# Performance work log

Measured on AMD Instinct MI355X. Metric: run time of the kernel, lower is better.

## Reference

```python
import jax, jax.numpy as jnp
import numpy as np

B, S = 32, 4096
QRYDIM, CTXDIM, ENCDIM = 512, 512, 256


def setup_inputs() -> dict:
    key = jax.random.key(0)
    ks = jax.random.split(key, 8)
    qry = jax.random.normal(ks[0], (B, QRYDIM), dtype=jnp.float32)
    ctx = jax.random.normal(ks[1], (B, S, CTXDIM), dtype=jnp.float32)
    ctx_mask = jax.random.randint(ks[2], (B, S), 0, 2, dtype=jnp.int32)
    # first Linear(qrydim+ctxdim, encdim): split into ctx-part and qry-part
    # (equivalent to concat([ctx, qry]) @ W1^T since concat order is [ctx, qry])
    sc1 = 1.0 / np.sqrt(QRYDIM + CTXDIM)
    Wc = jax.random.uniform(ks[3], (CTXDIM, ENCDIM), jnp.float32, -sc1, sc1)
    Wq = jax.random.uniform(ks[4], (QRYDIM, ENCDIM), jnp.float32, -sc1, sc1)
    b1 = jax.random.uniform(ks[5], (ENCDIM,), jnp.float32, -sc1, sc1)
    sc2 = 1.0 / np.sqrt(ENCDIM)
    w2 = jax.random.uniform(ks[6], (ENCDIM,), jnp.float32, -sc2, sc2)
    b2 = jax.random.uniform(ks[7], (), jnp.float32, -sc2, sc2)
    return {"qry": qry, "ctx": ctx, "ctx_mask": ctx_mask,
            "Wc": Wc, "Wq": Wq, "b1": b1, "w2": w2, "b2": b2}


def reference(qry, ctx, ctx_mask, Wc, Wq, b1, w2, b2):
    # hidden = tanh(concat([ctx, qry_broadcast]) @ W1 + b1), computed without
    # materializing the (B, S, CTXDIM+QRYDIM) concat tensor
    h_ctx = jnp.einsum('bsc,ce->bse', ctx, Wc)          # (B, S, E)
    h_qry = jnp.einsum('bq,qe->be', qry, Wq)            # (B, E)
    h = jnp.tanh(h_ctx + h_qry[:, None, :] + b1)        # (B, S, E)
    scores = jnp.einsum('bse,e->bs', h, w2) + b2        # (B, S)
    # additive log-mask, then softmax over seqlen
    scores = scores + jnp.log(ctx_mask.astype(jnp.float32))
    alphas = jax.nn.softmax(scores, axis=-1)            # (B, S)
    # weighted sum over context (values default to ctx)
    summary = jnp.einsum('bs,bsd->bd', alphas, ctx)     # (B, CTXDIM)
    return alphas, summary, scores
```

## Files before the change

kernel.cpp:

```cpp
#include <hip/hip_runtime.h>
#include <math.h>

#define BB 32
#define SS 4096
#define CD 512
#define ED 256

#define ALPHAS_OFF 0
#define SUMMARY_OFF (BB * SS)
#define SCORES_OFF (BB * SS + BB * CD)

#define NEG_BIG (-1.0e30f)

typedef __attribute__((ext_vector_type(8))) short short8;
typedef __attribute__((ext_vector_type(8))) unsigned short us8;
typedef __attribute__((ext_vector_type(4))) float f32x4;

__device__ __forceinline__ unsigned short f2bf(float f) {
    unsigned u = __float_as_uint(f);
    u += 0x7FFFu + ((u >> 16) & 1u);
    return (unsigned short)(u >> 16);
}
__device__ __forceinline__ float bf2f(unsigned short h) {
    return __uint_as_float(((unsigned)h) << 16);
}
__device__ __forceinline__ float fast_tanh(float x) {
    const float ex = __expf(2.0f * x);
    return 1.0f - __fdividef(2.0f, ex + 1.0f);
}

#define WS_BH_OFF 32768
#define BPLANE 131072

__global__ void k_prep(const float* __restrict__ Wc, unsigned short* __restrict__ Bh,
                       unsigned short* __restrict__ Bl) {
    const int bid = blockIdx.x;
    const int l = threadIdx.x;
    const int e = (bid & 15) * 16 + (l & 15);
    const int kbase = (bid >> 4) * 32 + (l >> 4) * 8;
    const size_t off = ((size_t)bid * 64 + l) * 8;
#pragma unroll
    for (int j = 0; j < 8; ++j) {
        const float f = Wc[(size_t)(kbase + j) * ED + e];
        const unsigned short h = f2bf(f);
        Bh[off + j] = h;
        Bl[off + j] = f2bf(f - bf2f(h));
    }
}

__global__ void k_hq(const float* __restrict__ qry, const float* __restrict__ Wq,
                     const float* __restrict__ b1, float* __restrict__ hq) {
    const int b = blockIdx.x;
    const int e = threadIdx.x;
    __shared__ float qs[CD];
    qs[e] = qry[b * CD + e];
    qs[e + 256] = qry[b * CD + e + 256];
    __syncthreads();
    float acc = b1[e];
#pragma unroll 8
    for (int c = 0; c < CD; ++c) {
        acc = fmaf(qs[c], Wq[c * ED + e], acc);
    }
    hq[b * ED + e] = acc;
}

#define ST 64
__global__ __launch_bounds__(256, 3)
void k_scores(const float* __restrict__ ctx,
              const unsigned short* __restrict__ Bh, const unsigned short* __restrict__ Bl,
              const float* __restrict__ hq, const float* __restrict__ w2,
              const float* __restrict__ b2p, const int* __restrict__ mask,
              float* __restrict__ out) {
    const int b = blockIdx.y;
    const int s0 = blockIdx.x * ST;
    const int tid = threadIdx.x;
    const int w = tid >> 6;
    const int l = tid & 63;
    const int ehalf = w & 1;
    const int mhalf = w >> 1;

    __shared__ unsigned short AsH[4 * 64 * 8];
    __shared__ unsigned short AsL[4 * 64 * 8];
    __shared__ unsigned short BsH[16 * 64 * 8];
    __shared__ unsigned short BsL[16 * 64 * 8];
    __shared__ float red[2][ST];

    f32x4 acc[2][8];
#pragma unroll
    for (int mi = 0; mi < 2; ++mi)
#pragma unroll
        for (int t = 0; t < 8; ++t) acc[mi][t] = (f32x4)(0.0f);

    const float* ctx_b = ctx + (size_t)(b * SS + s0) * CD;

    for (int c = 0; c < 16; ++c) {
        __syncthreads();
#pragma unroll
        for (int i = 0; i < 2; ++i) {
            const int f = tid + i * 256;
            const int r = f >> 3;
            const int kk = (f & 7) * 4;
            const float4 v = *(const float4*)(ctx_b + (size_t)r * CD + c * 32 + kk);
            const unsigned short h0 = f2bf(v.x), h1 = f2bf(v.y), h2 = f2bf(v.z), h3 = f2bf(v.w);
            const ushort4 hv = make_ushort4(h0, h1, h2, h3);
            const ushort4 lv = make_ushort4(f2bf(v.x - bf2f(h0)), f2bf(v.y - bf2f(h1)),
                                            f2bf(v.z - bf2f(h2)), f2bf(v.w - bf2f(h3)));
            const int off = (((r >> 4) * 64) + (r & 15) + 16 * (kk >> 3)) * 8 + (kk & 7);
            *(ushort4*)(&AsH[off]) = hv;
            *(ushort4*)(&AsL[off]) = lv;
        }
        {
            const us8* gh = (const us8*)(Bh + (size_t)c * 8192);
            const us8* gl2 = (const us8*)(Bl + (size_t)c * 8192);
            us8* lh = (us8*)BsH;
            us8* ll = (us8*)BsL;
#pragma unroll
            for (int i = 0; i < 4; ++i) lh[tid + i * 256] = gh[tid + i * 256];
#pragma unroll
            for (int i = 0; i < 4; ++i) ll[tid + i * 256] = gl2[tid + i * 256];
        }
        __syncthreads();

        short8 ah[2], alr[2];
#pragma unroll
        for (int mi = 0; mi < 2; ++mi) {
            const int aoff = ((mhalf * 2 + mi) * 64 + l) * 8;
            ah[mi] = *(const short8*)(&AsH[aoff]);
            alr[mi] = *(const short8*)(&AsL[aoff]);
        }
#pragma unroll
        for (int et = 0; et < 8; ++et) {
            const int etile = ehalf * 8 + et;
            const int boff = (etile * 64 + l) * 8;
            const short8 bh = *(const short8*)(&BsH[boff]);
            const short8 bl = *(const short8*)(&BsL[boff]);
#pragma unroll
            for (int mi = 0; mi < 2; ++mi) {
                acc[mi][et] = __builtin_amdgcn_mfma_f32_16x16x32_bf16(ah[mi], bh, acc[mi][et], 0, 0, 0);
                acc[mi][et] = __builtin_amdgcn_mfma_f32_16x16x32_bf16(alr[mi], bh, acc[mi][et], 0, 0, 0);
                acc[mi][et] = __builtin_amdgcn_mfma_f32_16x16x32_bf16(ah[mi], bl, acc[mi][et], 0, 0, 0);
            }
        }
    }

    float hqr[8], w2r[8];
#pragma unroll
    for (int t = 0; t < 8; ++t) {
        const int e = (ehalf * 8 + t) * 16 + (l & 15);
        hqr[t] = hq[b * ED + e];
        w2r[t] = w2[e];
    }

#pragma unroll
    for (int mi = 0; mi < 2; ++mi) {
#pragma unroll
        for (int reg = 0; reg < 4; ++reg) {
            float v = 0.0f;
#pragma unroll
            for (int t = 0; t < 8; ++t) {
                v += w2r[t] * fast_tanh(acc[mi][t][reg] + hqr[t]);
            }
            v += __shfl_xor(v, 1, 64);
            v += __shfl_xor(v, 2, 64);
            v += __shfl_xor(v, 4, 64);
            v += __shfl_xor(v, 8, 64);
            if ((l & 15) == 0) {
                const int row = (l >> 4) * 4 + reg;
                red[ehalf][(mhalf * 2 + mi) * 16 + row] = v;
            }
        }
    }
    __syncthreads();
    if (tid < ST) {
        const int s = s0 + tid;
        float sc = red[0][tid] + red[1][tid] + b2p[0];
        if (mask[b * SS + s] == 0) sc = NEG_BIG;
        out[SCORES_OFF + b * SS + s] = sc;
    }
}

__global__ void k_softmax(float* __restrict__ out) {
    const int b = blockIdx.x;
    const int tid = threadIdx.x;
    const float* sc = out + SCORES_OFF + b * SS;
    float* al = out + ALPHAS_OFF + b * SS;

    __shared__ float red[4];
    __shared__ float bcast;
    const int lane = tid & 63;
    const int wave = tid >> 6;

    float loc[16];
    float mx = -INFINITY;
#pragma unroll
    for (int i = 0; i < 16; ++i) {
        loc[i] = sc[i * 256 + tid];
        mx = fmaxf(mx, loc[i]);
    }
    for (int off = 32; off >= 1; off >>= 1) mx = fmaxf(mx, __shfl_down(mx, off, 64));
    if (lane == 0) red[wave] = mx;
    __syncthreads();
    if (tid == 0) bcast = fmaxf(fmaxf(red[0], red[1]), fmaxf(red[2], red[3]));
    __syncthreads();
    const float mxall = bcast;

    float sum = 0.0f;
#pragma unroll
    for (int i = 0; i < 16; ++i) {
        const float ev = __expf(loc[i] - mxall);
        loc[i] = ev;
        sum += ev;
    }
    for (int off = 32; off >= 1; off >>= 1) sum += __shfl_down(sum, off, 64);
    if (lane == 0) red[wave] = sum;
    __syncthreads();
    if (tid == 0) bcast = red[0] + red[1] + red[2] + red[3];
    __syncthreads();
    const float inv = 1.0f / bcast;

#pragma unroll
    for (int i = 0; i < 16; ++i) al[i * 256 + tid] = loc[i] * inv;
}

__global__ void k_zero(float* __restrict__ out) {
    const int i = blockIdx.x * blockDim.x + threadIdx.x;
    if (i < BB * CD) out[SUMMARY_OFF + i] = 0.0f;
}

#define SROWS 128
__global__ void k_summary(const float* __restrict__ ctx, const float* __restrict__ out_alphas,
                          float* __restrict__ out) {
    const int b = blockIdx.y;
    const int s0 = blockIdx.x * SROWS;
    const int t = threadIdx.x;
    const int sg = t >> 7;
    const int d = (t & 127) * 4;

    __shared__ float al[SROWS];
    if (t < SROWS) al[t] = out_alphas[ALPHAS_OFF + b * SS + s0 + t];
    __syncthreads();

    const float* base = ctx + (size_t)(b * SS + s0 + sg * 64) * CD + d;
    const float* alp = &al[sg * 64];
    float4 a0 = make_float4(0.f, 0.f, 0.f, 0.f);
    float4 a1 = a0, a2 = a0, a3 = a0;
#pragma unroll 4
    for (int i = 0; i < 16; ++i) {
        const int s = i * 4;
        const float4 v0 = *(const float4*)(base + (size_t)(s + 0) * CD);
        const float4 v1 = *(const float4*)(base + (size_t)(s + 1) * CD);
        const float4 v2 = *(const float4*)(base + (size_t)(s + 2) * CD);
        const float4 v3 = *(const float4*)(base + (size_t)(s + 3) * CD);
        const float w0 = alp[s + 0], w1 = alp[s + 1], w2_ = alp[s + 2], w3 = alp[s + 3];
        a0.x = fmaf(w0, v0.x, a0.x); a0.y = fmaf(w0, v0.y, a0.y);
        a0.z = fmaf(w0, v0.z, a0.z); a0.w = fmaf(w0, v0.w, a0.w);
        a1.x = fmaf(w1, v1.x, a1.x); a1.y = fmaf(w1, v1.y, a1.y);
        a1.z = fmaf(w1, v1.z, a1.z); a1.w = fmaf(w1, v1.w, a1.w);
        a2.x = fmaf(w2_, v2.x, a2.x); a2.y = fmaf(w2_, v2.y, a2.y);
        a2.z = fmaf(w2_, v2.z, a2.z); a2.w = fmaf(w2_, v2.w, a2.w);
        a3.x = fmaf(w3, v3.x, a3.x); a3.y = fmaf(w3, v3.y, a3.y);
        a3.z = fmaf(w3, v3.z, a3.z); a3.w = fmaf(w3, v3.w, a3.w);
    }
    const float rx = (a0.x + a1.x) + (a2.x + a3.x);
    const float ry = (a0.y + a1.y) + (a2.y + a3.y);
    const float rz = (a0.z + a1.z) + (a2.z + a3.z);
    const float rw = (a0.w + a1.w) + (a2.w + a3.w);
    float* dst = out + SUMMARY_OFF + b * CD + d;
    atomicAdd(dst + 0, rx);
    atomicAdd(dst + 1, ry);
    atomicAdd(dst + 2, rz);
    atomicAdd(dst + 3, rw);
}

extern "C" void kernel_launch(void* const* d_in, const int* in_sizes, int n_in,
                              void* d_out, int out_size, void* d_ws, size_t ws_size,
                              hipStream_t stream) {
    const float* qry  = (const float*)d_in[0];
    const float* ctx  = (const float*)d_in[1];
    const int*   msk  = (const int*)d_in[2];
    const float* Wc   = (const float*)d_in[3];
    const float* Wq   = (const float*)d_in[4];
    const float* b1   = (const float*)d_in[5];
    const float* w2   = (const float*)d_in[6];
    const float* b2   = (const float*)d_in[7];
    float* out = (float*)d_out;
    float* hq = (float*)d_ws;
    unsigned short* Bh = (unsigned short*)((char*)d_ws + WS_BH_OFF);
    unsigned short* Bl = Bh + BPLANE;

    k_prep<<<256, 64, 0, stream>>>(Wc, Bh, Bl);
    k_hq<<<BB, ED, 0, stream>>>(qry, Wq, b1, hq);
    k_scores<<<dim3(SS / ST, BB), 256, 0, stream>>>(ctx, Bh, Bl, hq, w2, b2, msk, out);
    k_softmax<<<BB, 256, 0, stream>>>(out);
    k_zero<<<(BB * CD + 255) / 256, 256, 0, stream>>>(out);
    k_summary<<<dim3(SS / SROWS, BB), 256, 0, stream>>>(ctx, out, out);
}
```

Measured before the change: 489.1 us.

## Double scores tile to 128 rows with 512 threads; skip masked rows in summary

The scores kernel now processes 128 sequence rows per block with 8 waves. Each block loads the split-bf16 Wc chunk into shared memory once for twice as many rows, which halves B-tile traffic per row. The ctx staging now has each thread write one 8-element fragment directly in MFMA layout, replacing two 4-element scattered writes. The summary kernel skips loading ctx rows whose alpha is zero (masked positions), cutting memory reads for the roughly half of rows that are masked, at the cost of branchy, divergent loads. Higher launch bounds (512, 6) may constrain registers and could cause spills.

```diff
diff --git a/kernel.cpp b/kernel.cpp
--- a/kernel.cpp
+++ b/kernel.cpp
@@ -64,8 +64,8 @@
     hq[b * ED + e] = acc;
 }
 
-#define ST 64
-__global__ __launch_bounds__(256, 3)
+#define ST 128
+__global__ __launch_bounds__(512, 6)
 void k_scores(const float* __restrict__ ctx,
               const unsigned short* __restrict__ Bh, const unsigned short* __restrict__ Bl,
               const float* __restrict__ hq, const float* __restrict__ w2,
@@ -77,10 +77,10 @@
     const int w = tid >> 6;
     const int l = tid & 63;
     const int ehalf = w & 1;
-    const int mhalf = w >> 1;
-
-    __shared__ unsigned short AsH[4 * 64 * 8];
-    __shared__ unsigned short AsL[4 * 64 * 8];
+    const int mbase = (w >> 1) * 2;
+
+    __shared__ unsigned short AsH[8 * 64 * 8];
+    __shared__ unsigned short AsL[8 * 64 * 8];
     __shared__ unsigned short BsH[16 * 64 * 8];
     __shared__ unsigned short BsL[16 * 64 * 8];
     __shared__ float red[2][ST];
@@ -93,38 +93,44 @@
 
     const float* ctx_b = ctx + (size_t)(b * SS + s0) * CD;
 
+    const int amt = tid >> 6;
+    const int alif = tid & 63;
+    const int ar = amt * 16 + (alif & 15);
+    const int akg = alif >> 4;
+    const float* aptr = ctx_b + (size_t)ar * CD + akg * 8;
+
     for (int c = 0; c < 16; ++c) {
         __syncthreads();
-#pragma unroll
-        for (int i = 0; i < 2; ++i) {
-            const int f = tid + i * 256;
-            const int r = f >> 3;
-            const int kk = (f & 7) * 4;
-            const float4 v = *(const float4*)(ctx_b + (size_t)r * CD + c * 32 + kk);
-            const unsigned short h0 = f2bf(v.x), h1 = f2bf(v.y), h2 = f2bf(v.z), h3 = f2bf(v.w);
-            const ushort4 hv = make_ushort4(h0, h1, h2, h3);
-            const ushort4 lv = make_ushort4(f2bf(v.x - bf2f(h0)), f2bf(v.y - bf2f(h1)),
-                                            f2bf(v.z - bf2f(h2)), f2bf(v.w - bf2f(h3)));
-            const int off = (((r >> 4) * 64) + (r & 15) + 16 * (kk >> 3)) * 8 + (kk & 7);
-            *(ushort4*)(&AsH[off]) = hv;
-            *(ushort4*)(&AsL[off]) = lv;
+        {
+            const float4 v0 = *(const float4*)(aptr + c * 32);
+            const float4 v1 = *(const float4*)(aptr + c * 32 + 4);
+            const float f[8] = {v0.x, v0.y, v0.z, v0.w, v1.x, v1.y, v1.z, v1.w};
+            us8 H, L;
+#pragma unroll
+            for (int j = 0; j < 8; ++j) {
+                const unsigned short h = f2bf(f[j]);
+                H[j] = h;
+                L[j] = f2bf(f[j] - bf2f(h));
+            }
+            *(us8*)(&AsH[tid * 8]) = H;
+            *(us8*)(&AsL[tid * 8]) = L;
         }
         {
             const us8* gh = (const us8*)(Bh + (size_t)c * 8192);
             const us8* gl2 = (const us8*)(Bl + (size_t)c * 8192);
             us8* lh = (us8*)BsH;
             us8* ll = (us8*)BsL;
-#pragma unroll
-            for (int i = 0; i < 4; ++i) lh[tid + i * 256] = gh[tid + i * 256];
-#pragma unroll
-            for (int i = 0; i < 4; ++i) ll[tid + i * 256] = gl2[tid + i * 256];
+            lh[tid] = gh[tid];
+            lh[tid + 512] = gh[tid + 512];
+            ll[tid] = gl2[tid];
+            ll[tid + 512] = gl2[tid + 512];
         }
         __syncthreads();
 
         short8 ah[2], alr[2];
 #pragma unroll
         for (int mi = 0; mi < 2; ++mi) {
-            const int aoff = ((mhalf * 2 + mi) * 64 + l) * 8;
+            const int aoff = ((mbase + mi) * 64 + l) * 8;
             ah[mi] = *(const short8*)(&AsH[aoff]);
             alr[mi] = *(const short8*)(&AsL[aoff]);
         }
@@ -166,7 +172,7 @@
             v += __shfl_xor(v, 8, 64);
             if ((l & 15) == 0) {
                 const int row = (l >> 4) * 4 + reg;
-                red[ehalf][(mhalf * 2 + mi) * 16 + row] = v;
+                red[ehalf][(mbase + mi) * 16 + row] = v;
             }
         }
     }
@@ -244,22 +250,30 @@
     const float* alp = &al[sg * 64];
     float4 a0 = make_float4(0.f, 0.f, 0.f, 0.f);
     float4 a1 = a0, a2 = a0, a3 = a0;
-#pragma unroll 4
+#pragma unroll 2
     for (int i = 0; i < 16; ++i) {
         const int s = i * 4;
-        const float4 v0 = *(const float4*)(base + (size_t)(s + 0) * CD);
-        const float4 v1 = *(const float4*)(base + (size_t)(s + 1) * CD);
-        const float4 v2 = *(const float4*)(base + (size_t)(s + 2) * CD);
-        const float4 v3 = *(const float4*)(base + (size_t)(s + 3) * CD);
         const float w0 = alp[s + 0], w1 = alp[s + 1], w2_ = alp[s + 2], w3 = alp[s + 3];
-        a0.x = fmaf(w0, v0.x, a0.x); a0.y = fmaf(w0, v0.y, a0.y);
-        a0.z = fmaf(w0, v0.z, a0.z); a0.w = fmaf(w0, v0.w, a0.w);
-        a1.x = fmaf(w1, v1.x, a1.x); a1.y = fmaf(w1, v1.y, a1.y);
-        a1.z = fmaf(w1, v1.z, a1.z); a1.w = fmaf(w1, v1.w, a1.w);
-        a2.x = fmaf(w2_, v2.x, a2.x); a2.y = fmaf(w2_, v2.y, a2.y);
-        a2.z = fmaf(w2_, v2.z, a2.z); a2.w = fmaf(w2_, v2.w, a2.w);
-        a3.x = fmaf(w3, v3.x, a3.x); a3.y = fmaf(w3, v3.y, a3.y);
-        a3.z = fmaf(w3, v3.z, a3.z); a3.w = fmaf(w3, v3.w, a3.w);
+        if (w0 != 0.0f) {
+            const float4 v0 = *(const float4*)(base + (size_t)(s + 0) * CD);
+            a0.x = fmaf(w0, v0.x, a0.x); a0.y = fmaf(w0, v0.y, a0.y);
+            a0.z = fmaf(w0, v0.z, a0.z); a0.w = fmaf(w0, v0.w, a0.w);
+        }
+        if (w1 != 0.0f) {
+            const float4 v1 = *(const float4*)(base + (size_t)(s + 1) * CD);
+            a1.x = fmaf(w1, v1.x, a1.x); a1.y = fmaf(w1, v1.y, a1.y);
+            a1.z = fmaf(w1, v1.z, a1.z); a1.w = fmaf(w1, v1.w, a1.w);
+        }
+        if (w2_ != 0.0f) {
+            const float4 v2 = *(const float4*)(base + (size_t)(s + 2) * CD);
+            a2.x = fmaf(w2_, v2.x, a2.x); a2.y = fmaf(w2_, v2.y, a2.y);
+            a2.z = fmaf(w2_, v2.z, a2.z); a2.w = fmaf(w2_, v2.w, a2.w);
+        }
+        if (w3 != 0.0f) {
+            const float4 v3 = *(const float4*)(base + (size_t)(s + 3) * CD);
+            a3.x = fmaf(w3, v3.x, a3.x); a3.y = fmaf(w3, v3.y, a3.y);
+            a3.z = fmaf(w3, v3.z, a3.z); a3.w = fmaf(w3, v3.w, a3.w);
+        }
     }
     const float rx = (a0.x + a1.x) + (a2.x + a3.x);
     const float ry = (a0.y + a1.y) + (a2.y + a3.y);
@@ -290,7 +304,7 @@
 
     k_prep<<<256, 64, 0, stream>>>(Wc, Bh, Bl);
     k_hq<<<BB, ED, 0, stream>>>(qry, Wq, b1, hq);
-    k_scores<<<dim3(SS / ST, BB), 256, 0, stream>>>(ctx, Bh, Bl, hq, w2, b2, msk, out);
+    k_scores<<<dim3(SS / ST, BB), 512, 0, stream>>>(ctx, Bh, Bl, hq, w2, b2, msk, out);
     k_softmax<<<BB, 256, 0, stream>>>(out);
     k_zero<<<(BB * CD + 255) / 256, 256, 0, stream>>>(out);
     k_summary<<<dim3(SS / SROWS, BB), 256, 0, stream>>>(ctx, out, out);
```

New measurement: 825.0 us. +68.7%, slower.
